# Performance work log

Measured on AMD Instinct MI355X. Metric: run time of the kernel, lower is better.

## Reference

```python
import jax, jax.numpy as jnp
import numpy as np

N_NODES = 100000
N_EDGES = 1600000
D_FEAT = 32
D_HID = 64
D_OUT = 64


def setup_inputs() -> dict:
    key = jax.random.key(0)
    ks = jax.random.split(key, 7)
    x = jax.random.normal(ks[0], (N_NODES, D_FEAT), dtype=jnp.float32)
    pos = jax.random.uniform(ks[1], (N_NODES, 3), dtype=jnp.float32) * 100.0
    # Fixed-size stand-in for radius_graph(pos, 5) output: (2, E) [source; target]
    edge_index = jax.random.randint(ks[2], (2, N_EDGES), 0, N_NODES, dtype=jnp.int64)
    d_in = D_FEAT + 3  # concat(x_j, pos_j - pos_i)
    W1 = jax.random.normal(ks[3], (d_in, D_HID), dtype=jnp.float32) / np.sqrt(d_in)
    b1 = jnp.zeros((D_HID,), dtype=jnp.float32)
    W2 = jax.random.normal(ks[4], (D_HID, D_OUT), dtype=jnp.float32) / np.sqrt(D_HID)
    b2 = jnp.zeros((D_OUT,), dtype=jnp.float32)
    return {"x": x, "pos": pos, "edge_index": edge_index,
            "W1": W1, "b1": b1, "W2": W2, "b2": b2}


def reference(x, pos, edge_index, W1, b1, W2, b2):
    n = x.shape[0]
    # PointNetConv default add_self_loops=True (radius_graph used loop=False)
    loops = jnp.arange(n, dtype=edge_index.dtype)
    src = jnp.concatenate([edge_index[0], loops])  # source j
    dst = jnp.concatenate([edge_index[1], loops])  # target i
    # gather: per-edge message input [E+N, d_feat+3]
    msg_in = jnp.concatenate([x[src], pos[src] - pos[dst]], axis=-1)
    # local_nn MLP
    h = jax.nn.relu(msg_in @ W1 + b1) @ W2 + b2
    # scatter: max-aggregate onto target nodes (PointConv aggr='max')
    out = jax.ops.segment_max(h, dst, num_segments=n)
    return out
```

## Files before the change

### kernel.cpp

```cpp
#include <hip/hip_runtime.h>
#include <math.h>

#define N_NODES 100000
#define N_EDGES 1600000
#define D_FEAT 32
#define D_HID 64
#define D_OUT 64
#define CAP 48
#define NPB 32
#define NBKT 3125
#define B1 256
#define E_PER_B1 6250
#define NB_NODE 1024
#define AGG_B 2048

typedef _Float16 half8 __attribute__((ext_vector_type(8)));
typedef float f32x4  __attribute__((ext_vector_type(4)));

__device__ inline unsigned pk_subrelu(unsigned v, unsigned nq) {
    unsigned r;
    asm("v_pk_add_f16 %0, %1, %2\n\t"
        "v_pk_max_f16 %0, %0, 0"
        : "=v"(r) : "v"(v), "v"(nq));
    return r;
}

__global__ __launch_bounds__(256)
void node_kernel(const float* __restrict__ x,
                 const float* __restrict__ pos,
                 const float* __restrict__ W1,
                 const float* __restrict__ b1,
                 unsigned short* __restrict__ vb,
                 unsigned short* __restrict__ qb) {
    const int lane = threadIdx.x & 63;
    const int wid  = (blockIdx.x * blockDim.x + threadIdx.x) >> 6;
    const int nw   = (NB_NODE * 256) >> 6;

    float w[D_FEAT + 3];
#pragma unroll
    for (int f = 0; f < D_FEAT + 3; ++f)
        w[f] = W1[f * D_HID + lane];
    const float bb = b1[lane];

    for (int node = wid; node < N_NODES; node += nw) {
        const float* xr = x + (size_t)node * D_FEAT;
        float acc = bb;
#pragma unroll
        for (int f = 0; f < D_FEAT; ++f)
            acc = fmaf(xr[f], w[f], acc);

        const float* pr = pos + (size_t)node * 3;
        float qa = 0.0f;
#pragma unroll
        for (int p = 0; p < 3; ++p)
            qa = fmaf(pr[p], w[D_FEAT + p], qa);

        vb[(size_t)node * D_HID + lane] =
            __builtin_bit_cast(unsigned short, (_Float16)(acc + qa));
        qb[(size_t)node * D_HID + lane] =
            __builtin_bit_cast(unsigned short, (_Float16)(-qa));
    }
}

__global__ __launch_bounds__(1024)
void sort_kernel(const int* __restrict__ src,
                 const int* __restrict__ dst,
                 unsigned int* __restrict__ coarse,
                 int* __restrict__ dirT,
                 const float* __restrict__ W2,
                 unsigned short* __restrict__ W2T) {
    __shared__ int hist[NBKT];
    __shared__ int stage[E_PER_B1];
    __shared__ int wsum[16];

    const int tid  = threadIdx.x;
    const int lane = tid & 63;
    const int wv   = tid >> 6;
    const int e0   = blockIdx.x * E_PER_B1;

    if (blockIdx.x == 0) {
        for (int i = tid; i < D_HID * D_OUT; i += 1024) {
            float w = W2[i];
            W2T[(size_t)(i & 63) * D_HID + (i >> 6)] =
                __builtin_bit_cast(unsigned short, (_Float16)w);
        }
    }

    for (int b = tid; b < NBKT; b += 1024) hist[b] = 0;
    __syncthreads();

    for (int e = e0 + tid; e < e0 + E_PER_B1; e += 1024)
        atomicAdd(&hist[dst[e] >> 5], 1);
    __syncthreads();

    const int i0 = tid * 4;
    int c[4];
    int sum = 0;
#pragma unroll
    for (int k = 0; k < 4; ++k) {
        c[k] = (i0 + k < NBKT) ? hist[i0 + k] : 0;
        sum += c[k];
    }
    int inc = sum;
#pragma unroll
    for (int d = 1; d < 64; d <<= 1) {
        int u = __shfl_up(inc, d, 64);
        if (lane >= d) inc += u;
    }
    if (lane == 63) wsum[wv] = inc;
    __syncthreads();
    if (wv == 0) {
        int s = (lane < 16) ? wsum[lane] : 0;
#pragma unroll
        for (int d = 1; d < 16; d <<= 1) {
            int u = __shfl_up(s, d, 64);
            if (lane >= d) s += u;
        }
        if (lane < 16) wsum[lane] = s;
    }
    __syncthreads();
    int excl = inc - sum + ((wv > 0) ? wsum[wv - 1] : 0);
#pragma unroll
    for (int k = 0; k < 4; ++k) {
        if (i0 + k < NBKT) hist[i0 + k] = excl;
        excl += c[k];
    }
    __syncthreads();

    for (int b = tid; b < NBKT; b += 1024)
        dirT[(size_t)b * B1 + blockIdx.x] = e0 + hist[b];
    __syncthreads();

    for (int e = e0 + tid; e < e0 + E_PER_B1; e += 1024) {
        int d = dst[e], s = src[e];
        int p = atomicAdd(&hist[d >> 5], 1);
        stage[p] = (int)(((unsigned)s << 5) | (unsigned)(d & 31));
    }
    __syncthreads();

    for (int i = tid; i < E_PER_B1; i += 1024)
        coarse[e0 + i] = (unsigned)stage[i];
}

__global__ __launch_bounds__(256)
void agg_kernel(const unsigned short* __restrict__ vb,
                const unsigned short* __restrict__ qb,
                const unsigned short* __restrict__ W2T,
                const float* __restrict__ b2,
                const int* __restrict__ dirT,
                const unsigned int* __restrict__ coarse,
                int* __restrict__ ctr,
                float* __restrict__ out) {
    __shared__ int lcnt[NPB];
    __shared__ int lslots[NPB][CAP];
    __shared__ int sbkt;

    const int tid  = threadIdx.x;
    const int lane = tid & 63;
    const int wave = tid >> 6;
    const int quad = lane >> 4;
    const int mrow = lane & 15;

    half8 bfrag[4][2];
#pragma unroll
    for (int t = 0; t < 4; ++t)
#pragma unroll
        for (int kh = 0; kh < 2; ++kh)
            bfrag[t][kh] = *(const half8*)(W2T + (size_t)(t * 16 + mrow) * D_HID
                                               + kh * 32 + quad * 8);
    float bias[4];
#pragma unroll
    for (int t = 0; t < 4; ++t) bias[t] = b2[t * 16 + mrow];

    while (true) {
        if (tid == 0) sbkt = atomicAdd(ctr, 1);
        __syncthreads();
        const int bkt = sbkt;
        if (bkt >= NBKT) break;
        const int nbase = bkt << 5;

        for (int i = tid; i < NPB; i += 256) lcnt[i] = 0;
        __syncthreads();

        {
            const int s0 = dirT[(size_t)bkt * B1 + tid];
            const int s1 = (bkt + 1 < NBKT) ? dirT[(size_t)(bkt + 1) * B1 + tid]
                                            : (tid + 1) * E_PER_B1;
            for (int j = s0; j < s1; ++j) {
                unsigned enc = coarse[j];
                int local = (int)(enc & 31u);
                int s     = (int)(enc >> 5);
                int p = atomicAdd(&lcnt[local], 1);
                if (p < CAP) lslots[local][p] = s;
            }
        }
        __syncthreads();

        for (int ln = wave; ln < NPB; ln += 4) {
            const int node = nbase + ln;

            const uint4 nq0 = *(const uint4*)(qb + (size_t)node * D_HID + quad * 8);
            const uint4 nq1 = *(const uint4*)(qb + (size_t)node * D_HID + 32 + quad * 8);

            int deg = lcnt[ln];
            if (deg > CAP) deg = CAP;
            const int rows = deg + 1;
            const int nbat = (rows + 15) >> 4;

            float rmax[4][4];
#pragma unroll
            for (int t = 0; t < 4; ++t)
#pragma unroll
                for (int r = 0; r < 4; ++r) rmax[t][r] = -INFINITY;

            for (int b = 0; b < nbat; ++b) {
                int idx = b * 16 + mrow;
                int idxc = (idx < CAP) ? idx : (CAP - 1);
                int s = (idx < deg) ? lslots[ln][idxc] : node;

                const uint4 v0 = *(const uint4*)(vb + (size_t)s * D_HID + quad * 8);
                const uint4 v1 = *(const uint4*)(vb + (size_t)s * D_HID + 32 + quad * 8);

                uint4 a0u, a1u;
                a0u.x = pk_subrelu(v0.x, nq0.x);
                a0u.y = pk_subrelu(v0.y, nq0.y);
                a0u.z = pk_subrelu(v0.z, nq0.z);
                a0u.w = pk_subrelu(v0.w, nq0.w);
                a1u.x = pk_subrelu(v1.x, nq1.x);
                a1u.y = pk_subrelu(v1.y, nq1.y);
                a1u.z = pk_subrelu(v1.z, nq1.z);
                a1u.w = pk_subrelu(v1.w, nq1.w);
                half8 a0 = __builtin_bit_cast(half8, a0u);
                half8 a1 = __builtin_bit_cast(half8, a1u);

#pragma unroll
                for (int t = 0; t < 4; ++t) {
                    f32x4 acc = (f32x4){0.f, 0.f, 0.f, 0.f};
                    acc = __builtin_amdgcn_mfma_f32_16x16x32_f16(a0, bfrag[t][0], acc, 0, 0, 0);
                    acc = __builtin_amdgcn_mfma_f32_16x16x32_f16(a1, bfrag[t][1], acc, 0, 0, 0);
#pragma unroll
                    for (int r = 0; r < 4; ++r)
                        rmax[t][r] = fmaxf(rmax[t][r], acc[r]);
                }
            }

            float fin[4];
#pragma unroll
            for (int t = 0; t < 4; ++t) {
                float m = fmaxf(fmaxf(rmax[t][0], rmax[t][1]), fmaxf(rmax[t][2], rmax[t][3]));
                m = fmaxf(m, __shfl_xor(m, 16, 64));
                m = fmaxf(m, __shfl_xor(m, 32, 64));
                fin[t] = m + bias[t];
            }
            float r = (quad == 0) ? fin[0] : (quad == 1) ? fin[1] : (quad == 2) ? fin[2] : fin[3];
            out[(size_t)node * D_OUT + lane] = r;
        }
        __syncthreads();
    }
}

extern "C" void kernel_launch(void* const* d_in, const int* in_sizes, int n_in,
                              void* d_out, int out_size, void* d_ws, size_t ws_size,
                              hipStream_t stream) {
    const float* x   = (const float*)d_in[0];
    const float* pos = (const float*)d_in[1];
    const int*   ei  = (const int*)d_in[2];
    const float* W1  = (const float*)d_in[3];
    const float* b1  = (const float*)d_in[4];
    const float* W2  = (const float*)d_in[5];
    const float* b2  = (const float*)d_in[6];
    float* out = (float*)d_out;

    char* ws = (char*)d_ws;
    unsigned short* vb   = (unsigned short*)ws;
    unsigned short* qb   = (unsigned short*)(ws + 12800000);
    unsigned int* coarse = (unsigned int*)(ws + 25600000);
    int*            dirT = (int*)(ws + 32000000);
    unsigned short* W2T  = (unsigned short*)(ws + 35200000);
    int*            ctr  = (int*)(ws + 35208192);

    const int* src = ei;
    const int* dst = ei + N_EDGES;

    (void)hipMemsetAsync(ctr, 0, sizeof(int), stream);
    hipLaunchKernelGGL(sort_kernel, dim3(B1), dim3(1024), 0, stream,
                       src, dst, coarse, dirT, W2, W2T);
    hipLaunchKernelGGL(node_kernel, dim3(NB_NODE), dim3(256), 0, stream,
                       x, pos, W1, b1, vb, qb);
    hipLaunchKernelGGL(agg_kernel, dim3(AGG_B), dim3(256), 0, stream,
                       vb, qb, W2T, b2, dirT, coarse, ctr, out);
}
```

Before: 216.1 us.

## Launch one aggregation block per bucket and prefetch first two gather batches

Replaces the persistent agg_kernel, which fetched buckets from an atomic work counter, with a grid of one block per 32-node bucket. This drops the counter memset, the per-bucket atomic and two block barriers per iteration. It also issues the first two 16-row batches of neighbour-row loads up front, before any MFMA work, so their gather latency overlaps. In exchange, each block reloads the W2 fragments and bias, there are more block launches, and register pressure rises from holding the prefetched rows.

```diff
diff --git a/kernel.cpp b/kernel.cpp
--- a/kernel.cpp
+++ b/kernel.cpp
@@ -12,7 +12,6 @@
 #define B1 256
 #define E_PER_B1 6250
 #define NB_NODE 1024
-#define AGG_B 2048
 
 typedef _Float16 half8 __attribute__((ext_vector_type(8)));
 typedef float f32x4  __attribute__((ext_vector_type(4)));
@@ -149,17 +148,17 @@
                 const float* __restrict__ b2,
                 const int* __restrict__ dirT,
                 const unsigned int* __restrict__ coarse,
-                int* __restrict__ ctr,
                 float* __restrict__ out) {
     __shared__ int lcnt[NPB];
     __shared__ int lslots[NPB][CAP];
-    __shared__ int sbkt;
 
     const int tid  = threadIdx.x;
     const int lane = tid & 63;
     const int wave = tid >> 6;
     const int quad = lane >> 4;
     const int mrow = lane & 15;
+    const int bkt  = blockIdx.x;
+    const int nbase = bkt << 5;
 
     half8 bfrag[4][2];
 #pragma unroll
@@ -172,90 +171,135 @@
 #pragma unroll
     for (int t = 0; t < 4; ++t) bias[t] = b2[t * 16 + mrow];
 
-    while (true) {
-        if (tid == 0) sbkt = atomicAdd(ctr, 1);
-        __syncthreads();
-        const int bkt = sbkt;
-        if (bkt >= NBKT) break;
-        const int nbase = bkt << 5;
-
-        for (int i = tid; i < NPB; i += 256) lcnt[i] = 0;
-        __syncthreads();
+    for (int i = tid; i < NPB; i += 256) lcnt[i] = 0;
+    __syncthreads();
+    {
+        const int s0 = dirT[(size_t)bkt * B1 + tid];
+        const int s1 = (bkt + 1 < NBKT) ? dirT[(size_t)(bkt + 1) * B1 + tid]
+                                        : (tid + 1) * E_PER_B1;
+        for (int j = s0; j < s1; ++j) {
+            unsigned enc = coarse[j];
+            int local = (int)(enc & 31u);
+            int s     = (int)(enc >> 5);
+            int p = atomicAdd(&lcnt[local], 1);
+            if (p < CAP) lslots[local][p] = s;
+        }
+    }
+    __syncthreads();
+
+    for (int ln = wave; ln < NPB; ln += 4) {
+        const int node = nbase + ln;
+
+        int deg = lcnt[ln];
+        if (deg > CAP) deg = CAP;
+        const int rows = deg + 1;
+        const int nbat = (rows + 15) >> 4;
+
+        const int idx0 = mrow;
+        const int idx1 = 16 + mrow;
+        const int sA = (idx0 < deg) ? lslots[ln][idx0] : node;
+        const int sB = (idx1 < deg) ? lslots[ln][idx1] : node;
+
+        const uint4 nq0 = *(const uint4*)(qb + (size_t)node * D_HID + quad * 8);
+        const uint4 nq1 = *(const uint4*)(qb + (size_t)node * D_HID + 32 + quad * 8);
+        const uint4 vA0 = *(const uint4*)(vb + (size_t)sA * D_HID + quad * 8);
+        const uint4 vA1 = *(const uint4*)(vb + (size_t)sA * D_HID + 32 + quad * 8);
+        const uint4 vB0 = *(const uint4*)(vb + (size_t)sB * D_HID + quad * 8);
+        const uint4 vB1 = *(const uint4*)(vb + (size_t)sB * D_HID + 32 + quad * 8);
+
+        float rmax[4][4];
+#pragma unroll
+        for (int t = 0; t < 4; ++t)
+#pragma unroll
+            for (int r = 0; r < 4; ++r) rmax[t][r] = -INFINITY;
 
         {
-            const int s0 = dirT[(size_t)bkt * B1 + tid];
-            const int s1 = (bkt + 1 < NBKT) ? dirT[(size_t)(bkt + 1) * B1 + tid]
-                                            : (tid + 1) * E_PER_B1;
-            for (int j = s0; j < s1; ++j) {
-                unsigned enc = coarse[j];
-                int local = (int)(enc & 31u);
-                int s     = (int)(enc >> 5);
-                int p = atomicAdd(&lcnt[local], 1);
-                if (p < CAP) lslots[local][p] = s;
+            uint4 a0u, a1u;
+            a0u.x = pk_subrelu(vA0.x, nq0.x);
+            a0u.y = pk_subrelu(vA0.y, nq0.y);
+            a0u.z = pk_subrelu(vA0.z, nq0.z);
+            a0u.w = pk_subrelu(vA0.w, nq0.w);
+            a1u.x = pk_subrelu(vA1.x, nq1.x);
+            a1u.y = pk_subrelu(vA1.y, nq1.y);
+            a1u.z = pk_subrelu(vA1.z, nq1.z);
+            a1u.w = pk_subrelu(vA1.w, nq1.w);
+            half8 a0 = __builtin_bit_cast(half8, a0u);
+            half8 a1 = __builtin_bit_cast(half8, a1u);
+#pragma unroll
+            for (int t = 0; t < 4; ++t) {
+                f32x4 acc = (f32x4){0.f, 0.f, 0.f, 0.f};
+                acc = __builtin_amdgcn_mfma_f32_16x16x32_f16(a0, bfrag[t][0], acc, 0, 0, 0);
+                acc = __builtin_amdgcn_mfma_f32_16x16x32_f16(a1, bfrag[t][1], acc, 0, 0, 0);
+#pragma unroll
+                for (int r = 0; r < 4; ++r)
+                    rmax[t][r] = fmaxf(rmax[t][r], acc[r]);
             }
         }
-        __syncthreads();
-
-        for (int ln = wave; ln < NPB; ln += 4) {
-            const int node = nbase + ln;
-
-            const uint4 nq0 = *(const uint4*)(qb + (size_t)node * D_HID + quad * 8);
-            const uint4 nq1 = *(const uint4*)(qb + (size_t)node * D_HID + 32 + quad * 8);
-
-            int deg = lcnt[ln];
-            if (deg > CAP) deg = CAP;
-            const int rows = deg + 1;
-            const int nbat = (rows + 15) >> 4;
-
-            float rmax[4][4];
-#pragma unroll
-            for (int t = 0; t < 4; ++t)
-#pragma unroll
-                for (int r = 0; r < 4; ++r) rmax[t][r] = -INFINITY;
-
-            for (int b = 0; b < nbat; ++b) {
-                int idx = b * 16 + mrow;
-                int idxc = (idx < CAP) ? idx : (CAP - 1);
-                int s = (idx < deg) ? lslots[ln][idxc] : node;
-
-                const uint4 v0 = *(const uint4*)(vb + (size_t)s * D_HID + quad * 8);
-                const uint4 v1 = *(const uint4*)(vb + (size_t)s * D_HID + 32 + quad * 8);
-
-                uint4 a0u, a1u;
-                a0u.x = pk_subrelu(v0.x, nq0.x);
-                a0u.y = pk_subrelu(v0.y, nq0.y);
-                a0u.z = pk_subrelu(v0.z, nq0.z);
-                a0u.w = pk_subrelu(v0.w, nq0.w);
-                a1u.x = pk_subrelu(v1.x, nq1.x);
-                a1u.y = pk_subrelu(v1.y, nq1.y);
-                a1u.z = pk_subrelu(v1.z, nq1.z);
-                a1u.w = pk_subrelu(v1.w, nq1.w);
-                half8 a0 = __builtin_bit_cast(half8, a0u);
-                half8 a1 = __builtin_bit_cast(half8, a1u);
-
-#pragma unroll
-                for (int t = 0; t < 4; ++t) {
-                    f32x4 acc = (f32x4){0.f, 0.f, 0.f, 0.f};
-                    acc = __builtin_amdgcn_mfma_f32_16x16x32_f16(a0, bfrag[t][0], acc, 0, 0, 0);
-                    acc = __builtin_amdgcn_mfma_f32_16x16x32_f16(a1, bfrag[t][1], acc, 0, 0, 0);
-#pragma unroll
-                    for (int r = 0; r < 4; ++r)
-                        rmax[t][r] = fmaxf(rmax[t][r], acc[r]);
-                }
+
+        if (nbat > 1) {
+            uint4 a0u, a1u;
+            a0u.x = pk_subrelu(vB0.x, nq0.x);
+            a0u.y = pk_subrelu(vB0.y, nq0.y);
+            a0u.z = pk_subrelu(vB0.z, nq0.z);
+            a0u.w = pk_subrelu(vB0.w, nq0.w);
+            a1u.x = pk_subrelu(vB1.x, nq1.x);
+            a1u.y = pk_subrelu(vB1.y, nq1.y);
+            a1u.z = pk_subrelu(vB1.z, nq1.z);
+            a1u.w = pk_subrelu(vB1.w, nq1.w);
+            half8 a0 = __builtin_bit_cast(half8, a0u);
+            half8 a1 = __builtin_bit_cast(half8, a1u);
+#pragma unroll
+            for (int t = 0; t < 4; ++t) {
+                f32x4 acc = (f32x4){0.f, 0.f, 0.f, 0.f};
+                acc = __builtin_amdgcn_mfma_f32_16x16x32_f16(a0, bfrag[t][0], acc, 0, 0, 0);
+                acc = __builtin_amdgcn_mfma_f32_16x16x32_f16(a1, bfrag[t][1], acc, 0, 0, 0);
+#pragma unroll
+                for (int r = 0; r < 4; ++r)
+                    rmax[t][r] = fmaxf(rmax[t][r], acc[r]);
             }
-
-            float fin[4];
+        }
+
+        for (int b = 2; b < nbat; ++b) {
+            int idx = b * 16 + mrow;
+            int idxc = (idx < CAP) ? idx : (CAP - 1);
+            int s = (idx < deg) ? lslots[ln][idxc] : node;
+
+            const uint4 v0 = *(const uint4*)(vb + (size_t)s * D_HID + quad * 8);
+            const uint4 v1 = *(const uint4*)(vb + (size_t)s * D_HID + 32 + quad * 8);
+
+            uint4 a0u, a1u;
+            a0u.x = pk_subrelu(v0.x, nq0.x);
+            a0u.y = pk_subrelu(v0.y, nq0.y);
+            a0u.z = pk_subrelu(v0.z, nq0.z);
+            a0u.w = pk_subrelu(v0.w, nq0.w);
+            a1u.x = pk_subrelu(v1.x, nq1.x);
+            a1u.y = pk_subrelu(v1.y, nq1.y);
+            a1u.z = pk_subrelu(v1.z, nq1.z);
+            a1u.w = pk_subrelu(v1.w, nq1.w);
+            half8 a0 = __builtin_bit_cast(half8, a0u);
+            half8 a1 = __builtin_bit_cast(half8, a1u);
+
 #pragma unroll
             for (int t = 0; t < 4; ++t) {
-                float m = fmaxf(fmaxf(rmax[t][0], rmax[t][1]), fmaxf(rmax[t][2], rmax[t][3]));
-                m = fmaxf(m, __shfl_xor(m, 16, 64));
-                m = fmaxf(m, __shfl_xor(m, 32, 64));
-                fin[t] = m + bias[t];
+                f32x4 acc = (f32x4){0.f, 0.f, 0.f, 0.f};
+                acc = __builtin_amdgcn_mfma_f32_16x16x32_f16(a0, bfrag[t][0], acc, 0, 0, 0);
+                acc = __builtin_amdgcn_mfma_f32_16x16x32_f16(a1, bfrag[t][1], acc, 0, 0, 0);
+#pragma unroll
+                for (int r = 0; r < 4; ++r)
+                    rmax[t][r] = fmaxf(rmax[t][r], acc[r]);
             }
-            float r = (quad == 0) ? fin[0] : (quad == 1) ? fin[1] : (quad == 2) ? fin[2] : fin[3];
-            out[(size_t)node * D_OUT + lane] = r;
-        }
-        __syncthreads();
+        }
+
+        float fin[4];
+#pragma unroll
+        for (int t = 0; t < 4; ++t) {
+            float m = fmaxf(fmaxf(rmax[t][0], rmax[t][1]), fmaxf(rmax[t][2], rmax[t][3]));
+            m = fmaxf(m, __shfl_xor(m, 16, 64));
+            m = fmaxf(m, __shfl_xor(m, 32, 64));
+            fin[t] = m + bias[t];
+        }
+        float r = (quad == 0) ? fin[0] : (quad == 1) ? fin[1] : (quad == 2) ? fin[2] : fin[3];
+        out[(size_t)node * D_OUT + lane] = r;
     }
 }
 
@@ -277,16 +321,14 @@
     unsigned int* coarse = (unsigned int*)(ws + 25600000);
     int*            dirT = (int*)(ws + 32000000);
     unsigned short* W2T  = (unsigned short*)(ws + 35200000);
-    int*            ctr  = (int*)(ws + 35208192);
 
     const int* src = ei;
     const int* dst = ei + N_EDGES;
 
-    (void)hipMemsetAsync(ctr, 0, sizeof(int), stream);
     hipLaunchKernelGGL(sort_kernel, dim3(B1), dim3(1024), 0, stream,
                        src, dst, coarse, dirT, W2, W2T);
     hipLaunchKernelGGL(node_kernel, dim3(NB_NODE), dim3(256), 0, stream,
                        x, pos, W1, b1, vb, qb);
-    hipLaunchKernelGGL(agg_kernel, dim3(AGG_B), dim3(256), 0, stream,
-                       vb, qb, W2T, b2, dirT, coarse, ctr, out);
-}
+    hipLaunchKernelGGL(agg_kernel, dim3(NBKT), dim3(256), 0, stream,
+                       vb, qb, W2T, b2, dirT, coarse, out);
+}
```

After: 199.7 us. 7.6% less time.

## Use one block per bucket, drop atomic work queue, tile node features in LDS

Applied to the files above, without the earlier changes.

The aggregation kernel drops its persistent atomic-counter work queue and launches one block per 32-node bucket, which also removes the memset of the counter. The directory layout is transposed so the sort kernel writes rows per sort-block and the agg kernel reads them strided per thread. The node kernel now stages a 64-node tile of x and pos in shared memory instead of each wave reading rows directly from global memory. This costs more block launches and strided directory reads in agg, in exchange for no global atomics and no serialized bucket fetch.

```diff
diff --git a/kernel.cpp b/kernel.cpp
--- a/kernel.cpp
+++ b/kernel.cpp
@@ -11,8 +11,8 @@
 #define NBKT 3125
 #define B1 256
 #define E_PER_B1 6250
-#define NB_NODE 1024
-#define AGG_B 2048
+#define NTILE 64
+#define NB_NODE 1563
 
 typedef _Float16 half8 __attribute__((ext_vector_type(8)));
 typedef float f32x4  __attribute__((ext_vector_type(4)));
@@ -32,28 +32,39 @@
                  const float* __restrict__ b1,
                  unsigned short* __restrict__ vb,
                  unsigned short* __restrict__ qb) {
-    const int lane = threadIdx.x & 63;
-    const int wid  = (blockIdx.x * blockDim.x + threadIdx.x) >> 6;
-    const int nw   = (NB_NODE * 256) >> 6;
+    __shared__ float xs[NTILE * D_FEAT];
+    __shared__ float ps[NTILE * 3];
+
+    const int tid  = threadIdx.x;
+    const int lane = tid & 63;
+    const int wave = tid >> 6;
+
+    const int n0  = blockIdx.x * NTILE;
+    const int cnt = (N_NODES - n0 < NTILE) ? (N_NODES - n0) : NTILE;
+
+    for (int i = tid; i < cnt * D_FEAT; i += 256)
+        xs[i] = x[(size_t)n0 * D_FEAT + i];
+    for (int i = tid; i < cnt * 3; i += 256)
+        ps[i] = pos[(size_t)n0 * 3 + i];
 
     float w[D_FEAT + 3];
 #pragma unroll
     for (int f = 0; f < D_FEAT + 3; ++f)
         w[f] = W1[f * D_HID + lane];
     const float bb = b1[lane];
-
-    for (int node = wid; node < N_NODES; node += nw) {
-        const float* xr = x + (size_t)node * D_FEAT;
+    __syncthreads();
+
+    for (int ln = wave; ln < cnt; ln += 4) {
+        const int node = n0 + ln;
         float acc = bb;
 #pragma unroll
         for (int f = 0; f < D_FEAT; ++f)
-            acc = fmaf(xr[f], w[f], acc);
-
-        const float* pr = pos + (size_t)node * 3;
+            acc = fmaf(xs[ln * D_FEAT + f], w[f], acc);
+
         float qa = 0.0f;
 #pragma unroll
         for (int p = 0; p < 3; ++p)
-            qa = fmaf(pr[p], w[D_FEAT + p], qa);
+            qa = fmaf(ps[ln * 3 + p], w[D_FEAT + p], qa);
 
         vb[(size_t)node * D_HID + lane] =
             __builtin_bit_cast(unsigned short, (_Float16)(acc + qa));
@@ -66,7 +77,7 @@
 void sort_kernel(const int* __restrict__ src,
                  const int* __restrict__ dst,
                  unsigned int* __restrict__ coarse,
-                 int* __restrict__ dirT,
+                 int* __restrict__ dir,
                  const float* __restrict__ W2,
                  unsigned short* __restrict__ W2T) {
     __shared__ int hist[NBKT];
@@ -128,7 +139,7 @@
     __syncthreads();
 
     for (int b = tid; b < NBKT; b += 1024)
-        dirT[(size_t)b * B1 + blockIdx.x] = e0 + hist[b];
+        dir[(size_t)blockIdx.x * NBKT + b] = e0 + hist[b];
     __syncthreads();
 
     for (int e = e0 + tid; e < e0 + E_PER_B1; e += 1024) {
@@ -147,19 +158,19 @@
                 const unsigned short* __restrict__ qb,
                 const unsigned short* __restrict__ W2T,
                 const float* __restrict__ b2,
-                const int* __restrict__ dirT,
+                const int* __restrict__ dir,
                 const unsigned int* __restrict__ coarse,
-                int* __restrict__ ctr,
                 float* __restrict__ out) {
     __shared__ int lcnt[NPB];
     __shared__ int lslots[NPB][CAP];
-    __shared__ int sbkt;
 
     const int tid  = threadIdx.x;
     const int lane = tid & 63;
     const int wave = tid >> 6;
     const int quad = lane >> 4;
     const int mrow = lane & 15;
+    const int bkt  = blockIdx.x;
+    const int nbase = bkt << 5;
 
     half8 bfrag[4][2];
 #pragma unroll
@@ -172,90 +183,80 @@
 #pragma unroll
     for (int t = 0; t < 4; ++t) bias[t] = b2[t * 16 + mrow];
 
-    while (true) {
-        if (tid == 0) sbkt = atomicAdd(ctr, 1);
-        __syncthreads();
-        const int bkt = sbkt;
-        if (bkt >= NBKT) break;
-        const int nbase = bkt << 5;
-
-        for (int i = tid; i < NPB; i += 256) lcnt[i] = 0;
-        __syncthreads();
-
-        {
-            const int s0 = dirT[(size_t)bkt * B1 + tid];
-            const int s1 = (bkt + 1 < NBKT) ? dirT[(size_t)(bkt + 1) * B1 + tid]
-                                            : (tid + 1) * E_PER_B1;
-            for (int j = s0; j < s1; ++j) {
-                unsigned enc = coarse[j];
-                int local = (int)(enc & 31u);
-                int s     = (int)(enc >> 5);
-                int p = atomicAdd(&lcnt[local], 1);
-                if (p < CAP) lslots[local][p] = s;
+    for (int i = tid; i < NPB; i += 256) lcnt[i] = 0;
+    __syncthreads();
+    {
+        const int s0 = dir[(size_t)tid * NBKT + bkt];
+        const int s1 = (bkt + 1 < NBKT) ? dir[(size_t)tid * NBKT + bkt + 1]
+                                        : (tid + 1) * E_PER_B1;
+        for (int j = s0; j < s1; ++j) {
+            unsigned enc = coarse[j];
+            int local = (int)(enc & 31u);
+            int s     = (int)(enc >> 5);
+            int p = atomicAdd(&lcnt[local], 1);
+            if (p < CAP) lslots[local][p] = s;
+        }
+    }
+    __syncthreads();
+
+    for (int ln = wave; ln < NPB; ln += 4) {
+        const int node = nbase + ln;
+
+        const uint4 nq0 = *(const uint4*)(qb + (size_t)node * D_HID + quad * 8);
+        const uint4 nq1 = *(const uint4*)(qb + (size_t)node * D_HID + 32 + quad * 8);
+
+        int deg = lcnt[ln];
+        if (deg > CAP) deg = CAP;
+        const int rows = deg + 1;
+        const int nbat = (rows + 15) >> 4;
+
+        float rmax[4][4];
+#pragma unroll
+        for (int t = 0; t < 4; ++t)
+#pragma unroll
+            for (int r = 0; r < 4; ++r) rmax[t][r] = -INFINITY;
+
+        for (int b = 0; b < nbat; ++b) {
+            int idx = b * 16 + mrow;
+            int idxc = (idx < CAP) ? idx : (CAP - 1);
+            int s = (idx < deg) ? lslots[ln][idxc] : node;
+
+            const uint4 v0 = *(const uint4*)(vb + (size_t)s * D_HID + quad * 8);
+            const uint4 v1 = *(const uint4*)(vb + (size_t)s * D_HID + 32 + quad * 8);
+
+            uint4 a0u, a1u;
+            a0u.x = pk_subrelu(v0.x, nq0.x);
+            a0u.y = pk_subrelu(v0.y, nq0.y);
+            a0u.z = pk_subrelu(v0.z, nq0.z);
+            a0u.w = pk_subrelu(v0.w, nq0.w);
+            a1u.x = pk_subrelu(v1.x, nq1.x);
+            a1u.y = pk_subrelu(v1.y, nq1.y);
+            a1u.z = pk_subrelu(v1.z, nq1.z);
+            a1u.w = pk_subrelu(v1.w, nq1.w);
+            half8 a0 = __builtin_bit_cast(half8, a0u);
+            half8 a1 = __builtin_bit_cast(half8, a1u);
+
+#pragma unroll
+            for (int t = 0; t < 4; ++t) {
+                f32x4 acc = (f32x4){0.f, 0.f, 0.f, 0.f};
+                acc = __builtin_amdgcn_mfma_f32_16x16x32_f16(a0, bfrag[t][0], acc, 0, 0, 0);
+                acc = __builtin_amdgcn_mfma_f32_16x16x32_f16(a1, bfrag[t][1], acc, 0, 0, 0);
+#pragma unroll
+                for (int r = 0; r < 4; ++r)
+                    rmax[t][r] = fmaxf(rmax[t][r], acc[r]);
             }
         }
-        __syncthreads();
-
-        for (int ln = wave; ln < NPB; ln += 4) {
-            const int node = nbase + ln;
-
-            const uint4 nq0 = *(const uint4*)(qb + (size_t)node * D_HID + quad * 8);
-            const uint4 nq1 = *(const uint4*)(qb + (size_t)node * D_HID + 32 + quad * 8);
-
-            int deg = lcnt[ln];
-            if (deg > CAP) deg = CAP;
-            const int rows = deg + 1;
-            const int nbat = (rows + 15) >> 4;
-
-            float rmax[4][4];
-#pragma unroll
-            for (int t = 0; t < 4; ++t)
-#pragma unroll
-                for (int r = 0; r < 4; ++r) rmax[t][r] = -INFINITY;
-
-            for (int b = 0; b < nbat; ++b) {
-                int idx = b * 16 + mrow;
-                int idxc = (idx < CAP) ? idx : (CAP - 1);
-                int s = (idx < deg) ? lslots[ln][idxc] : node;
-
-                const uint4 v0 = *(const uint4*)(vb + (size_t)s * D_HID + quad * 8);
-                const uint4 v1 = *(const uint4*)(vb + (size_t)s * D_HID + 32 + quad * 8);
-
-                uint4 a0u, a1u;
-                a0u.x = pk_subrelu(v0.x, nq0.x);
-                a0u.y = pk_subrelu(v0.y, nq0.y);
-                a0u.z = pk_subrelu(v0.z, nq0.z);
-                a0u.w = pk_subrelu(v0.w, nq0.w);
-                a1u.x = pk_subrelu(v1.x, nq1.x);
-                a1u.y = pk_subrelu(v1.y, nq1.y);
-                a1u.z = pk_subrelu(v1.z, nq1.z);
-                a1u.w = pk_subrelu(v1.w, nq1.w);
-                half8 a0 = __builtin_bit_cast(half8, a0u);
-                half8 a1 = __builtin_bit_cast(half8, a1u);
-
-#pragma unroll
-                for (int t = 0; t < 4; ++t) {
-                    f32x4 acc = (f32x4){0.f, 0.f, 0.f, 0.f};
-                    acc = __builtin_amdgcn_mfma_f32_16x16x32_f16(a0, bfrag[t][0], acc, 0, 0, 0);
-                    acc = __builtin_amdgcn_mfma_f32_16x16x32_f16(a1, bfrag[t][1], acc, 0, 0, 0);
-#pragma unroll
-                    for (int r = 0; r < 4; ++r)
-                        rmax[t][r] = fmaxf(rmax[t][r], acc[r]);
-                }
-            }
-
-            float fin[4];
-#pragma unroll
-            for (int t = 0; t < 4; ++t) {
-                float m = fmaxf(fmaxf(rmax[t][0], rmax[t][1]), fmaxf(rmax[t][2], rmax[t][3]));
-                m = fmaxf(m, __shfl_xor(m, 16, 64));
-                m = fmaxf(m, __shfl_xor(m, 32, 64));
-                fin[t] = m + bias[t];
-            }
-            float r = (quad == 0) ? fin[0] : (quad == 1) ? fin[1] : (quad == 2) ? fin[2] : fin[3];
-            out[(size_t)node * D_OUT + lane] = r;
-        }
-        __syncthreads();
+
+        float fin[4];
+#pragma unroll
+        for (int t = 0; t < 4; ++t) {
+            float m = fmaxf(fmaxf(rmax[t][0], rmax[t][1]), fmaxf(rmax[t][2], rmax[t][3]));
+            m = fmaxf(m, __shfl_xor(m, 16, 64));
+            m = fmaxf(m, __shfl_xor(m, 32, 64));
+            fin[t] = m + bias[t];
+        }
+        float r = (quad == 0) ? fin[0] : (quad == 1) ? fin[1] : (quad == 2) ? fin[2] : fin[3];
+        out[(size_t)node * D_OUT + lane] = r;
     }
 }
 
@@ -275,18 +276,16 @@
     unsigned short* vb   = (unsigned short*)ws;
     unsigned short* qb   = (unsigned short*)(ws + 12800000);
     unsigned int* coarse = (unsigned int*)(ws + 25600000);
-    int*            dirT = (int*)(ws + 32000000);
+    int*            dir  = (int*)(ws + 32000000);
     unsigned short* W2T  = (unsigned short*)(ws + 35200000);
-    int*            ctr  = (int*)(ws + 35208192);
 
     const int* src = ei;
     const int* dst = ei + N_EDGES;
 
-    (void)hipMemsetAsync(ctr, 0, sizeof(int), stream);
     hipLaunchKernelGGL(sort_kernel, dim3(B1), dim3(1024), 0, stream,
-                       src, dst, coarse, dirT, W2, W2T);
+                       src, dst, coarse, dir, W2, W2T);
     hipLaunchKernelGGL(node_kernel, dim3(NB_NODE), dim3(256), 0, stream,
                        x, pos, W1, b1, vb, qb);
-    hipLaunchKernelGGL(agg_kernel, dim3(AGG_B), dim3(256), 0, stream,
-                       vb, qb, W2T, b2, dirT, coarse, ctr, out);
-}
+    hipLaunchKernelGGL(agg_kernel, dim3(NBKT), dim3(256), 0, stream,
+                       vb, qb, W2T, b2, dir, coarse, out);
+}
```

Result: faster. 182.0 us (-15.8%).
